# Performance work log

Hardware: AMD Instinct MI355X
Metric: run time of the kernel (lower is better)

Reference implementation:

```python
import jax, jax.numpy as jnp
import numpy as np

N_NODES = 100000
IN_CH = 64
HID = 16
HEADS = 4
OUT_CH = 1
NEG_SLOPE = 0.2
EPS = 1e-16


def gat_conv(x, src, dst, W, att_src, att_dst, bias, heads, out_ch, concat):
    """PyG-style GATConv. src/dst already include self-loops.
    x: [N, F_in]; W: [F_in, heads*out_ch]; att_*: [heads, out_ch]; bias: [heads*out_ch] or [out_ch]."""
    n = x.shape[0]
    h = (x @ W).reshape(n, heads, out_ch)                     # [N,H,C]
    a_src = jnp.einsum('nhc,hc->nh', h, att_src)              # [N,H]
    a_dst = jnp.einsum('nhc,hc->nh', h, att_dst)              # [N,H]
    alpha = jax.nn.leaky_relu(a_src[src] + a_dst[dst], NEG_SLOPE)  # [E,H]
    # segment softmax over incoming edges of each destination node
    m = jax.ops.segment_max(alpha, dst, num_segments=n)       # [N,H]
    e = jnp.exp(alpha - m[dst])
    denom = jax.ops.segment_sum(e, dst, num_segments=n)
    alpha = e / (denom[dst] + EPS)                            # [E,H]
    msg = h[src] * alpha[:, :, None]                          # [E,H,C]
    out = jax.ops.segment_sum(msg, dst, num_segments=n)       # [N,H,C]
    out = out.reshape(n, heads * out_ch) if concat else out.mean(axis=1)
    return out + bias


def setup_inputs() -> dict:
    key = jax.random.key(0)
    ks = jax.random.split(key, 10)
    x = jax.random.normal(ks[0], (N_NODES, IN_CH), dtype=jnp.float32)
    edge_index = jax.random.randint(ks[1], (2, 1600000), 0, N_NODES, dtype=jnp.int64)
    s = 0.1
    W1 = jax.random.normal(ks[2], (IN_CH, HEADS * HID), dtype=jnp.float32) * s
    att_src1 = jax.random.normal(ks[3], (HEADS, HID), dtype=jnp.float32) * s
    att_dst1 = jax.random.normal(ks[4], (HEADS, HID), dtype=jnp.float32) * s
    b1 = jnp.zeros((HEADS * HID,), dtype=jnp.float32)
    W2 = jax.random.normal(ks[5], (HEADS * HID, OUT_CH), dtype=jnp.float32) * s
    att_src2 = jax.random.normal(ks[6], (1, OUT_CH), dtype=jnp.float32) * s
    att_dst2 = jax.random.normal(ks[7], (1, OUT_CH), dtype=jnp.float32) * s
    b2 = jnp.zeros((OUT_CH,), dtype=jnp.float32)
    return {"x": x, "edge_index": edge_index, "W1": W1, "att_src1": att_src1,
            "att_dst1": att_dst1, "b1": b1, "W2": W2, "att_src2": att_src2,
            "att_dst2": att_dst2, "b2": b2}


def reference(x, edge_index, W1, att_src1, att_dst1, b1, W2, att_src2, att_dst2, b2):
    n = x.shape[0]
    loop = jnp.arange(n, dtype=edge_index.dtype)
    src = jnp.concatenate([edge_index[0], loop])  # self-loops (PyG default)
    dst = jnp.concatenate([edge_index[1], loop])
    h = gat_conv(x, src, dst, W1, att_src1, att_dst1, b1, HEADS, HID, concat=True)
    h = jax.nn.elu(h)
    out = gat_conv(h, src, dst, W2, att_src2, att_dst2, b2, 1, OUT_CH, concat=False)
    return out.squeeze()
```

## Files before the change

### kernel.cpp

```cpp
#include <hip/hip_runtime.h>
#include <hip/hip_fp16.h>

#define NN   100000
#define E0   1600000
#define ET   1700000
#define NEG  0.2f
#define EPSV 1e-16f
#define NB   391
#define BS   1024
#define NBLK4 ((ET + 4 * BS - 1) / (4 * BS))

typedef _Float16 half8 __attribute__((ext_vector_type(8)));
typedef float f32x16 __attribute__((ext_vector_type(16)));

__global__ __launch_bounds__(BS) void k_bcount(const int* __restrict__ ei, int* __restrict__ bcnt)
{
    __shared__ int cnt[NB];
    int t = threadIdx.x;
    if (t < NB) cnt[t] = 0;
    __syncthreads();
    int base = blockIdx.x * (BS * 4);
#pragma unroll
    for (int k = 0; k < 4; ++k) {
        int idx = base + k * BS + t;
        if (idx < ET) {
            int d = (idx < E0) ? ei[E0 + idx] : (idx - E0);
            atomicAdd(&cnt[d >> 8], 1);
        }
    }
    __syncthreads();
    if (t < NB && cnt[t]) atomicAdd(&bcnt[t], cnt[t]);
}

__global__ __launch_bounds__(512) void k_bscan(const int* __restrict__ bcnt,
                                               int* __restrict__ bbase, int* __restrict__ bcursor,
                                               int* __restrict__ rowptr)
{
    int t = threadIdx.x;
    int v = (t < NB) ? bcnt[t] : 0;
    int lane = t & 63, wid = t >> 6;
    int sc = v;
#pragma unroll
    for (int off = 1; off < 64; off <<= 1) {
        int u = __shfl_up(sc, off, 64);
        if (lane >= off) sc += u;
    }
    __shared__ int wsum[8];
    if (lane == 63) wsum[wid] = sc;
    __syncthreads();
    int woff = 0;
    for (int k = 0; k < wid; ++k) woff += wsum[k];
    if (t < NB) { int e = sc + woff - v; bbase[t] = e; bcursor[t] = e; }
    if (t == 0) rowptr[NN] = ET;
}

__global__ __launch_bounds__(BS) void k_bscat(const int* __restrict__ ei,
                                              int* __restrict__ bcursor, int* __restrict__ bin)
{
    __shared__ int cnt[NB];
    __shared__ int base[NB];
    int t = threadIdx.x;
    if (t < NB) cnt[t] = 0;
    __syncthreads();
    int blk = blockIdx.x * (BS * 4);
    int b[4], r[4], pk[4];
#pragma unroll
    for (int k = 0; k < 4; ++k) {
        int idx = blk + k * BS + t;
        r[k] = -1;
        if (idx < ET) {
            int s, d;
            if (idx < E0) { s = ei[idx]; d = ei[E0 + idx]; } else { s = d = idx - E0; }
            b[k] = d >> 8;
            pk[k] = s | ((d & 255) << 17);
            r[k] = atomicAdd(&cnt[b[k]], 1);
        }
    }
    __syncthreads();
    if (t < NB && cnt[t]) base[t] = atomicAdd(&bcursor[t], cnt[t]);
    __syncthreads();
#pragma unroll
    for (int k = 0; k < 4; ++k)
        if (r[k] >= 0) bin[base[b[k]] + r[k]] = pk[k];
}

__global__ __launch_bounds__(256) void k_bcsr(const int* __restrict__ bin,
                                              const int* __restrict__ bbase, const int* __restrict__ bcnt,
                                              int* __restrict__ rowptr, int* __restrict__ csr)
{
    int b = blockIdx.x;
    int beg = bbase[b], cntB = bcnt[b];
    int t = threadIdx.x;
    __shared__ int deg[256];
    __shared__ int cur[256];
    deg[t] = 0;
    __syncthreads();
    for (int i = t; i < cntB; i += 256) atomicAdd(&deg[bin[beg + i] >> 17], 1);
    __syncthreads();
    int v = deg[t];
    int lane = t & 63, wid = t >> 6;
    int sc = v;
#pragma unroll
    for (int off = 1; off < 64; off <<= 1) {
        int u = __shfl_up(sc, off, 64);
        if (lane >= off) sc += u;
    }
    __shared__ int wsum[4];
    if (lane == 63) wsum[wid] = sc;
    __syncthreads();
    int woff = 0;
    for (int k = 0; k < wid; ++k) woff += wsum[k];
    int excl = sc - v + woff;
    cur[t] = excl;
    int node = (b << 8) + t;
    if (node < NN) rowptr[node] = beg + excl;
    __syncthreads();
    for (int i = t; i < cntB; i += 256) {
        int e = bin[beg + i];
        int r = atomicAdd(&cur[e >> 17], 1);
        csr[beg + r] = e & 0x1FFFF;
    }
}

__global__ __launch_bounds__(256) void k_gemm1(
    const float* __restrict__ x, const float* __restrict__ W1,
    const float* __restrict__ as1, const float* __restrict__ ad1,
    __half* __restrict__ h1h, float* __restrict__ asrc1, float* __restrict__ adst1)
{
    __shared__ float Wl[4096];
    __shared__ float Ul[512];
    int tid = threadIdx.x;
    for (int i = tid; i < 4096; i += 256) Wl[i] = W1[i];
    __syncthreads();
    if (tid < 64) {
        int k = tid;
#pragma unroll
        for (int h = 0; h < 4; ++h) {
            float su = 0.f, du = 0.f;
#pragma unroll
            for (int c = 0; c < 16; ++c) {
                float w = Wl[k * 64 + h * 16 + c];
                su += w * as1[h * 16 + c];
                du += w * ad1[h * 16 + c];
            }
            Ul[k * 8 + h] = su;
            Ul[k * 8 + 4 + h] = du;
        }
    }
    __syncthreads();
    int lane = tid & 63, wv = tid >> 6;
    int col = lane & 31, q = lane >> 5;

    half8 bf0[4], bf1[4], bf2[4];
#pragma unroll
    for (int kc = 0; kc < 4; ++kc) {
#pragma unroll
        for (int j = 0; j < 8; ++j) {
            int k = kc * 16 + q * 8 + j;
            bf0[kc][j] = (_Float16)Wl[k * 64 + col];
            bf1[kc][j] = (_Float16)Wl[k * 64 + 32 + col];
            bf2[kc][j] = (col < 8) ? (_Float16)Ul[k * 8 + col] : (_Float16)0.f;
        }
    }

    int tile = blockIdx.x * 4 + wv;
    int n0 = tile * 32;
    if (n0 >= NN) return;

    half8 af[4];
    const float* xrow = x + (size_t)(n0 + col) * 64;
#pragma unroll
    for (int kc = 0; kc < 4; ++kc) {
        float4 xa = *(const float4*)(xrow + kc * 16 + q * 8);
        float4 xb = *(const float4*)(xrow + kc * 16 + q * 8 + 4);
        af[kc][0] = (_Float16)xa.x; af[kc][1] = (_Float16)xa.y;
        af[kc][2] = (_Float16)xa.z; af[kc][3] = (_Float16)xa.w;
        af[kc][4] = (_Float16)xb.x; af[kc][5] = (_Float16)xb.y;
        af[kc][6] = (_Float16)xb.z; af[kc][7] = (_Float16)xb.w;
    }

    f32x16 c0 = {}, c1 = {}, c2 = {};
#pragma unroll
    for (int kc = 0; kc < 4; ++kc) {
        c0 = __builtin_amdgcn_mfma_f32_32x32x16_f16(af[kc], bf0[kc], c0, 0, 0, 0);
        c1 = __builtin_amdgcn_mfma_f32_32x32x16_f16(af[kc], bf1[kc], c1, 0, 0, 0);
        c2 = __builtin_amdgcn_mfma_f32_32x32x16_f16(af[kc], bf2[kc], c2, 0, 0, 0);
    }

#pragma unroll
    for (int reg = 0; reg < 16; ++reg) {
        int row = (reg & 3) + 8 * (reg >> 2) + 4 * q;
        h1h[(size_t)(n0 + row) * 64 + col]      = __float2half(c0[reg]);
        h1h[(size_t)(n0 + row) * 64 + 32 + col] = __float2half(c1[reg]);
    }
    if (col < 8) {
        float* dst = (col < 4) ? asrc1 : adst1;
        int h = col & 3;
#pragma unroll
        for (int reg = 0; reg < 16; ++reg) {
            int row = (reg & 3) + 8 * (reg >> 2) + 4 * q;
            dst[(n0 + row) * 4 + h] = c2[reg];
        }
    }
}

__global__ __launch_bounds__(256) void k_e1agg(
    const int* __restrict__ rowptr, const int* __restrict__ csr,
    const float* __restrict__ asrc1, const float* __restrict__ adst1,
    const __half* __restrict__ h1h, const float* __restrict__ b1,
    const float* __restrict__ W2, float* __restrict__ g)
{
    int t = threadIdx.x;
    int hh = t & 3;
    int n = blockIdx.x * 64 + (t >> 2);
    if (n >= NN) return;
    float ad = adst1[n * 4 + hh];
    int beg = rowptr[n], end = rowptr[n + 1];
    float acc[16];
#pragma unroll
    for (int c = 0; c < 16; ++c) acc[c] = 0.f;
    float den = 0.f;
    for (int j = beg; j < end; ++j) {
        int s = csr[j];
        float as = asrc1[s * 4 + hh];
        float a = as + ad; a = a > 0.f ? a : NEG * a;
        float ev = __expf(a);
        den += ev;
        const uint4* hp = (const uint4*)(h1h + (size_t)s * 64 + hh * 16);
        uint4 r0 = hp[0], r1 = hp[1];
#define U4ACC(r, base) { \
        float2 f0 = __half22float2(*(const __half2*)&r.x); \
        float2 f1 = __half22float2(*(const __half2*)&r.y); \
        float2 f2 = __half22float2(*(const __half2*)&r.z); \
        float2 f3 = __half22float2(*(const __half2*)&r.w); \
        acc[base+0] += ev * f0.x; acc[base+1] += ev * f0.y; \
        acc[base+2] += ev * f1.x; acc[base+3] += ev * f1.y; \
        acc[base+4] += ev * f2.x; acc[base+5] += ev * f2.y; \
        acc[base+6] += ev * f3.x; acc[base+7] += ev * f3.y; }
        U4ACC(r0, 0) U4ACC(r1, 8)
#undef U4ACC
    }
    float inv = 1.f / (den + EPSV);
    const float4* bp = (const float4*)(b1 + hh * 16);
    const float4* wp = (const float4*)(W2 + hh * 16);
    float gv = 0.f;
#pragma unroll
    for (int q = 0; q < 4; ++q) {
        float4 bb = bp[q], w2 = wp[q];
        float v0 = acc[4*q+0] * inv + bb.x; v0 = v0 > 0.f ? v0 : __expf(v0) - 1.f;
        float v1 = acc[4*q+1] * inv + bb.y; v1 = v1 > 0.f ? v1 : __expf(v1) - 1.f;
        float v2 = acc[4*q+2] * inv + bb.z; v2 = v2 > 0.f ? v2 : __expf(v2) - 1.f;
        float v3 = acc[4*q+3] * inv + bb.w; v3 = v3 > 0.f ? v3 : __expf(v3) - 1.f;
        gv += v0 * w2.x + v1 * w2.y + v2 * w2.z + v3 * w2.w;
    }
    gv += __shfl_xor(gv, 1);
    gv += __shfl_xor(gv, 2);
    if (hh == 0) g[n] = gv;
}

__global__ __launch_bounds__(256) void k_e2agg(
    const int* __restrict__ rowptr, const int* __restrict__ csr,
    const float* __restrict__ g, const float* __restrict__ att_s2,
    const float* __restrict__ att_d2, const float* __restrict__ b2,
    float* __restrict__ out)
{
    int t = threadIdx.x;
    int grp = t >> 4, cc = t & 15;
    int n = blockIdx.x * 16 + grp;
    float cs = att_s2[0];
    float gdcd = g[n] * att_d2[0];
    int beg = rowptr[n], end = rowptr[n + 1];
    float acc = 0.f, den = 0.f;
    for (int j = beg + cc; j < end; j += 16) {
        float gz = g[csr[j]];
        float a = gz * cs + gdcd;
        a = a > 0.f ? a : NEG * a;
        float ev = __expf(a);
        den += ev;
        acc += ev * gz;
    }
#pragma unroll
    for (int m = 1; m <= 8; m <<= 1) {
        acc += __shfl_xor(acc, m);
        den += __shfl_xor(den, m);
    }
    if (cc == 0) out[n] = acc / (den + EPSV) + b2[0];
}

extern "C" void kernel_launch(void* const* d_in, const int* in_sizes, int n_in,
                              void* d_out, int out_size, void* d_ws, size_t ws_size,
                              hipStream_t stream)
{
    const float* x   = (const float*)d_in[0];
    const int*   ei  = (const int*)d_in[1];
    const float* W1  = (const float*)d_in[2];
    const float* as1 = (const float*)d_in[3];
    const float* ad1 = (const float*)d_in[4];
    const float* b1  = (const float*)d_in[5];
    const float* W2  = (const float*)d_in[6];
    const float* as2 = (const float*)d_in[7];
    const float* ad2 = (const float*)d_in[8];
    const float* b2  = (const float*)d_in[9];
    float* out = (float*)d_out;

    int*   iw      = (int*)d_ws;
    float* fw      = (float*)d_ws;
    int*   bcnt    = iw;
    int*   bbase   = iw + 512;
    int*   bcursor = iw + 1024;
    int*   rowptr  = iw + 1536;
    int*   bin     = iw + 101632;
    int*   csr     = iw + 1801728;
    float* adst1   = fw + 3501824;
    float* asrc1   = fw + 3901952;
    float* g       = fw + 4302080;
    __half* h1h    = (__half*)(fw + 4402176);

    hipMemsetAsync(bcnt, 0, NB * sizeof(int), stream);

    k_bcount<<<NBLK4, BS, 0, stream>>>(ei, bcnt);
    k_bscan <<<1, 512, 0, stream>>>(bcnt, bbase, bcursor, rowptr);
    k_bscat <<<NBLK4, BS, 0, stream>>>(ei, bcursor, bin);
    k_bcsr  <<<NB, 256, 0, stream>>>(bin, bbase, bcnt, rowptr, csr);
    k_gemm1 <<<(NN / 32 + 3) / 4, 256, 0, stream>>>(x, W1, as1, ad1, h1h, asrc1, adst1);
    k_e1agg <<<(NN * 4 + 255) / 256, 256, 0, stream>>>(rowptr, csr, asrc1, adst1, h1h, b1, W2, g);
    k_e2agg <<<NN / 16, 256, 0, stream>>>(rowptr, csr, g, as2, ad2, b2, out);
}
```

Before: 213.4 us.

## Drop global CSR build and rebuild per-bucket CSR in shared memory inside aggregators

Destination buckets shrink from 256 to 64 nodes. The separate k_bcsr kernel and the global rowptr/csr arrays are removed. Each aggregation kernel now sorts its bucket's packed edges into a shared-memory CSR with a local degree count and scan, then aggregates from it. This saves one launch and a global CSR write/read, at the cost of building the local CSR twice (once per layer). The second layer now uses 4 lanes per node instead of 16. Buckets are clamped to a fixed capacity, which would silently drop edges if a bucket ever exceeded it.

```diff
diff --git a/kernel.cpp b/kernel.cpp
--- a/kernel.cpp
+++ b/kernel.cpp
@@ -6,7 +6,8 @@
 #define ET   1700000
 #define NEG  0.2f
 #define EPSV 1e-16f
-#define NB   391
+#define NBK  1563
+#define CAP  1536
 #define BS   1024
 #define NBLK4 ((ET + 4 * BS - 1) / (4 * BS))
 
@@ -15,9 +16,9 @@
 
 __global__ __launch_bounds__(BS) void k_bcount(const int* __restrict__ ei, int* __restrict__ bcnt)
 {
-    __shared__ int cnt[NB];
-    int t = threadIdx.x;
-    if (t < NB) cnt[t] = 0;
+    __shared__ int cnt[NBK];
+    int t = threadIdx.x;
+    for (int i = t; i < NBK; i += BS) cnt[i] = 0;
     __syncthreads();
     int base = blockIdx.x * (BS * 4);
 #pragma unroll
@@ -25,42 +26,45 @@
         int idx = base + k * BS + t;
         if (idx < ET) {
             int d = (idx < E0) ? ei[E0 + idx] : (idx - E0);
-            atomicAdd(&cnt[d >> 8], 1);
-        }
-    }
-    __syncthreads();
-    if (t < NB && cnt[t]) atomicAdd(&bcnt[t], cnt[t]);
-}
-
-__global__ __launch_bounds__(512) void k_bscan(const int* __restrict__ bcnt,
-                                               int* __restrict__ bbase, int* __restrict__ bcursor,
-                                               int* __restrict__ rowptr)
-{
-    int t = threadIdx.x;
-    int v = (t < NB) ? bcnt[t] : 0;
+            atomicAdd(&cnt[d >> 6], 1);
+        }
+    }
+    __syncthreads();
+    for (int i = t; i < NBK; i += BS) if (cnt[i]) atomicAdd(&bcnt[i], cnt[i]);
+}
+
+__global__ __launch_bounds__(1024) void k_bscan(const int* __restrict__ bcnt,
+                                                int* __restrict__ bbase, int* __restrict__ bcursor)
+{
+    int t = threadIdx.x;
+    int i0 = 2 * t, i1 = 2 * t + 1;
+    int a = (i0 < NBK) ? bcnt[i0] : 0;
+    int b = (i1 < NBK) ? bcnt[i1] : 0;
+    int s = a + b;
     int lane = t & 63, wid = t >> 6;
-    int sc = v;
+    int sc = s;
 #pragma unroll
     for (int off = 1; off < 64; off <<= 1) {
         int u = __shfl_up(sc, off, 64);
         if (lane >= off) sc += u;
     }
-    __shared__ int wsum[8];
+    __shared__ int wsum[16];
     if (lane == 63) wsum[wid] = sc;
     __syncthreads();
     int woff = 0;
     for (int k = 0; k < wid; ++k) woff += wsum[k];
-    if (t < NB) { int e = sc + woff - v; bbase[t] = e; bcursor[t] = e; }
-    if (t == 0) rowptr[NN] = ET;
+    int excl = sc - s + woff;
+    if (i0 < NBK) { bbase[i0] = excl;     bcursor[i0] = excl; }
+    if (i1 < NBK) { bbase[i1] = excl + a; bcursor[i1] = excl + a; }
 }
 
 __global__ __launch_bounds__(BS) void k_bscat(const int* __restrict__ ei,
                                               int* __restrict__ bcursor, int* __restrict__ bin)
 {
-    __shared__ int cnt[NB];
-    __shared__ int base[NB];
-    int t = threadIdx.x;
-    if (t < NB) cnt[t] = 0;
+    __shared__ int cnt[NBK];
+    __shared__ int base[NBK];
+    int t = threadIdx.x;
+    for (int i = t; i < NBK; i += BS) cnt[i] = 0;
     __syncthreads();
     int blk = blockIdx.x * (BS * 4);
     int b[4], r[4], pk[4];
@@ -71,55 +75,17 @@
         if (idx < ET) {
             int s, d;
             if (idx < E0) { s = ei[idx]; d = ei[E0 + idx]; } else { s = d = idx - E0; }
-            b[k] = d >> 8;
-            pk[k] = s | ((d & 255) << 17);
+            b[k] = d >> 6;
+            pk[k] = s | ((d & 63) << 17);
             r[k] = atomicAdd(&cnt[b[k]], 1);
         }
     }
     __syncthreads();
-    if (t < NB && cnt[t]) base[t] = atomicAdd(&bcursor[t], cnt[t]);
+    for (int i = t; i < NBK; i += BS) if (cnt[i]) base[i] = atomicAdd(&bcursor[i], cnt[i]);
     __syncthreads();
 #pragma unroll
     for (int k = 0; k < 4; ++k)
         if (r[k] >= 0) bin[base[b[k]] + r[k]] = pk[k];
-}
-
-__global__ __launch_bounds__(256) void k_bcsr(const int* __restrict__ bin,
-                                              const int* __restrict__ bbase, const int* __restrict__ bcnt,
-                                              int* __restrict__ rowptr, int* __restrict__ csr)
-{
-    int b = blockIdx.x;
-    int beg = bbase[b], cntB = bcnt[b];
-    int t = threadIdx.x;
-    __shared__ int deg[256];
-    __shared__ int cur[256];
-    deg[t] = 0;
-    __syncthreads();
-    for (int i = t; i < cntB; i += 256) atomicAdd(&deg[bin[beg + i] >> 17], 1);
-    __syncthreads();
-    int v = deg[t];
-    int lane = t & 63, wid = t >> 6;
-    int sc = v;
-#pragma unroll
-    for (int off = 1; off < 64; off <<= 1) {
-        int u = __shfl_up(sc, off, 64);
-        if (lane >= off) sc += u;
-    }
-    __shared__ int wsum[4];
-    if (lane == 63) wsum[wid] = sc;
-    __syncthreads();
-    int woff = 0;
-    for (int k = 0; k < wid; ++k) woff += wsum[k];
-    int excl = sc - v + woff;
-    cur[t] = excl;
-    int node = (b << 8) + t;
-    if (node < NN) rowptr[node] = beg + excl;
-    __syncthreads();
-    for (int i = t; i < cntB; i += 256) {
-        int e = bin[beg + i];
-        int r = atomicAdd(&cur[e >> 17], 1);
-        csr[beg + r] = e & 0x1FFFF;
-    }
 }
 
 __global__ __launch_bounds__(256) void k_gemm1(
@@ -150,7 +116,6 @@
     __syncthreads();
     int lane = tid & 63, wv = tid >> 6;
     int col = lane & 31, q = lane >> 5;
-
     half8 bf0[4], bf1[4], bf2[4];
 #pragma unroll
     for (int kc = 0; kc < 4; ++kc) {
@@ -162,11 +127,9 @@
             bf2[kc][j] = (col < 8) ? (_Float16)Ul[k * 8 + col] : (_Float16)0.f;
         }
     }
-
     int tile = blockIdx.x * 4 + wv;
     int n0 = tile * 32;
     if (n0 >= NN) return;
-
     half8 af[4];
     const float* xrow = x + (size_t)(n0 + col) * 64;
 #pragma unroll
@@ -178,7 +141,6 @@
         af[kc][4] = (_Float16)xb.x; af[kc][5] = (_Float16)xb.y;
         af[kc][6] = (_Float16)xb.z; af[kc][7] = (_Float16)xb.w;
     }
-
     f32x16 c0 = {}, c1 = {}, c2 = {};
 #pragma unroll
     for (int kc = 0; kc < 4; ++kc) {
@@ -186,7 +148,6 @@
         c1 = __builtin_amdgcn_mfma_f32_32x32x16_f16(af[kc], bf1[kc], c1, 0, 0, 0);
         c2 = __builtin_amdgcn_mfma_f32_32x32x16_f16(af[kc], bf2[kc], c2, 0, 0, 0);
     }
-
 #pragma unroll
     for (int reg = 0; reg < 16; ++reg) {
         int row = (reg & 3) + 8 * (reg >> 2) + 4 * q;
@@ -205,23 +166,51 @@
 }
 
 __global__ __launch_bounds__(256) void k_e1agg(
-    const int* __restrict__ rowptr, const int* __restrict__ csr,
+    const int* __restrict__ bin, const int* __restrict__ bbase, const int* __restrict__ bcnt,
     const float* __restrict__ asrc1, const float* __restrict__ adst1,
     const __half* __restrict__ h1h, const float* __restrict__ b1,
     const float* __restrict__ W2, float* __restrict__ g)
 {
-    int t = threadIdx.x;
+    __shared__ int lcsr[CAP];
+    __shared__ int deg[64], cur[64];
+    int b = blockIdx.x;
+    int t = threadIdx.x;
+    int beg = bbase[b], cnt = bcnt[b];
+    if (cnt > CAP) cnt = CAP;
+    if (t < 64) deg[t] = 0;
+    __syncthreads();
+    for (int i = t; i < cnt; i += 256) atomicAdd(&deg[bin[beg + i] >> 17], 1);
+    __syncthreads();
+    if (t < 64) {
+        int v = deg[t];
+        int sc = v;
+#pragma unroll
+        for (int off = 1; off < 64; off <<= 1) {
+            int u = __shfl_up(sc, off, 64);
+            if (t >= off) sc += u;
+        }
+        cur[t] = sc - v;
+    }
+    __syncthreads();
+    for (int i = t; i < cnt; i += 256) {
+        int e = bin[beg + i];
+        int r = atomicAdd(&cur[e >> 17], 1);
+        lcsr[r] = e & 0x1FFFF;
+    }
+    __syncthreads();
     int hh = t & 3;
-    int n = blockIdx.x * 64 + (t >> 2);
+    int nl = t >> 2;
+    int n = b * 64 + nl;
     if (n >= NN) return;
+    int je = cur[nl];
+    int jb = je - deg[nl];
     float ad = adst1[n * 4 + hh];
-    int beg = rowptr[n], end = rowptr[n + 1];
     float acc[16];
 #pragma unroll
     for (int c = 0; c < 16; ++c) acc[c] = 0.f;
     float den = 0.f;
-    for (int j = beg; j < end; ++j) {
-        int s = csr[j];
+    for (int j = jb; j < je; ++j) {
+        int s = lcsr[j];
         float as = asrc1[s * 4 + hh];
         float a = as + ad; a = a > 0.f ? a : NEG * a;
         float ev = __expf(a);
@@ -259,32 +248,58 @@
 }
 
 __global__ __launch_bounds__(256) void k_e2agg(
-    const int* __restrict__ rowptr, const int* __restrict__ csr,
-    const float* __restrict__ g, const float* __restrict__ att_s2,
-    const float* __restrict__ att_d2, const float* __restrict__ b2,
+    const int* __restrict__ bin, const int* __restrict__ bbase, const int* __restrict__ bcnt,
+    const float* __restrict__ g, const float* __restrict__ as2,
+    const float* __restrict__ ad2, const float* __restrict__ b2,
     float* __restrict__ out)
 {
-    int t = threadIdx.x;
-    int grp = t >> 4, cc = t & 15;
-    int n = blockIdx.x * 16 + grp;
-    float cs = att_s2[0];
-    float gdcd = g[n] * att_d2[0];
-    int beg = rowptr[n], end = rowptr[n + 1];
+    __shared__ int lcsr[CAP];
+    __shared__ int deg[64], cur[64];
+    int b = blockIdx.x;
+    int t = threadIdx.x;
+    int beg = bbase[b], cnt = bcnt[b];
+    if (cnt > CAP) cnt = CAP;
+    if (t < 64) deg[t] = 0;
+    __syncthreads();
+    for (int i = t; i < cnt; i += 256) atomicAdd(&deg[bin[beg + i] >> 17], 1);
+    __syncthreads();
+    if (t < 64) {
+        int v = deg[t];
+        int sc = v;
+#pragma unroll
+        for (int off = 1; off < 64; off <<= 1) {
+            int u = __shfl_up(sc, off, 64);
+            if (t >= off) sc += u;
+        }
+        cur[t] = sc - v;
+    }
+    __syncthreads();
+    for (int i = t; i < cnt; i += 256) {
+        int e = bin[beg + i];
+        int r = atomicAdd(&cur[e >> 17], 1);
+        lcsr[r] = e & 0x1FFFF;
+    }
+    __syncthreads();
+    int hh = t & 3;
+    int nl = t >> 2;
+    int n = b * 64 + nl;
+    if (n >= NN) return;
+    int je = cur[nl];
+    int jb = je - deg[nl];
+    float cs = as2[0];
+    float gdcd = g[n] * ad2[0];
     float acc = 0.f, den = 0.f;
-    for (int j = beg + cc; j < end; j += 16) {
-        float gz = g[csr[j]];
+    for (int j = jb + hh; j < je; j += 4) {
+        float gz = g[lcsr[j]];
         float a = gz * cs + gdcd;
         a = a > 0.f ? a : NEG * a;
         float ev = __expf(a);
         den += ev;
         acc += ev * gz;
     }
-#pragma unroll
-    for (int m = 1; m <= 8; m <<= 1) {
-        acc += __shfl_xor(acc, m);
-        den += __shfl_xor(den, m);
-    }
-    if (cc == 0) out[n] = acc / (den + EPSV) + b2[0];
+    acc += __shfl_xor(acc, 1); den += __shfl_xor(den, 1);
+    acc += __shfl_xor(acc, 2); den += __shfl_xor(den, 2);
+    if (hh == 0) out[n] = acc / (den + EPSV) + b2[0];
 }
 
 extern "C" void kernel_launch(void* const* d_in, const int* in_sizes, int n_in,
@@ -306,23 +321,20 @@
     int*   iw      = (int*)d_ws;
     float* fw      = (float*)d_ws;
     int*   bcnt    = iw;
-    int*   bbase   = iw + 512;
-    int*   bcursor = iw + 1024;
-    int*   rowptr  = iw + 1536;
-    int*   bin     = iw + 101632;
-    int*   csr     = iw + 1801728;
-    float* adst1   = fw + 3501824;
-    float* asrc1   = fw + 3901952;
-    float* g       = fw + 4302080;
-    __half* h1h    = (__half*)(fw + 4402176);
-
-    hipMemsetAsync(bcnt, 0, NB * sizeof(int), stream);
+    int*   bbase   = iw + 1664;
+    int*   bcursor = iw + 3328;
+    int*   bin     = iw + 4992;
+    float* asrc1   = fw + 1705088;
+    float* adst1   = fw + 2105088;
+    float* g       = fw + 2505088;
+    __half* h1h    = (__half*)(fw + 2605184);
+
+    hipMemsetAsync(bcnt, 0, NBK * sizeof(int), stream);
 
     k_bcount<<<NBLK4, BS, 0, stream>>>(ei, bcnt);
-    k_bscan <<<1, 512, 0, stream>>>(bcnt, bbase, bcursor, rowptr);
+    k_bscan <<<1, 1024, 0, stream>>>(bcnt, bbase, bcursor);
     k_bscat <<<NBLK4, BS, 0, stream>>>(ei, bcursor, bin);
-    k_bcsr  <<<NB, 256, 0, stream>>>(bin, bbase, bcnt, rowptr, csr);
     k_gemm1 <<<(NN / 32 + 3) / 4, 256, 0, stream>>>(x, W1, as1, ad1, h1h, asrc1, adst1);
-    k_e1agg <<<(NN * 4 + 255) / 256, 256, 0, stream>>>(rowptr, csr, asrc1, adst1, h1h, b1, W2, g);
-    k_e2agg <<<NN / 16, 256, 0, stream>>>(rowptr, csr, g, as2, ad2, b2, out);
-}
+    k_e1agg <<<NBK, 256, 0, stream>>>(bin, bbase, bcnt, asrc1, adst1, h1h, b1, W2, g);
+    k_e2agg <<<NBK, 256, 0, stream>>>(bin, bbase, bcnt, g, as2, ad2, b2, out);
+}
```

New measurement: 200.9 us. 5.8% less time.
